# Kernel tuning notes

Hardware: AMD Instinct MI355X
Metric: run time of the kernel (lower is better)

Reference implementation:

```python
import jax, jax.numpy as jnp
import numpy as np

H = 8
D_MODEL = 1024
D_K = D_MODEL // H
NEG = -1000000000.0


def layer_norm(x, a, b, eps=1e-06):
    # torch std: unbiased (ddof=1); module divides by (std + eps)
    mean = jnp.mean(x, axis=-1, keepdims=True)
    var = jnp.sum((x - mean) ** 2, axis=-1, keepdims=True) / (x.shape[-1] - 1)
    std = jnp.sqrt(var)
    return a * (x - mean) / (std + eps) + b


def setup_inputs() -> dict:
    key = jax.random.key(0)
    ks = jax.random.split(key, 12)
    B, S, D = 8, 1024, D_MODEL
    inp = {
        "query": jax.random.normal(ks[0], (B, S, D), jnp.float32),
        "value": jax.random.normal(ks[1], (B, S, D), jnp.float32),
        "key": jax.random.normal(ks[2], (B, S, D), jnp.float32),
        "mask": jax.random.randint(ks[3], (B, S), 0, 2, jnp.int32),
        "ln_a": jnp.ones((D,), jnp.float32),
        "ln_b": jnp.zeros((D,), jnp.float32),
        "wq": jax.random.normal(ks[4], (D, D), jnp.float32) * 0.02,
        "bq": jnp.zeros((D,), jnp.float32),
        "wk": jax.random.normal(ks[5], (D, D), jnp.float32) * 0.02,
        "bk": jnp.zeros((D,), jnp.float32),
        "wv": jax.random.normal(ks[6], (D, D), jnp.float32) * 0.02,
        "bv": jnp.zeros((D,), jnp.float32),
        "w_aoa": jax.random.normal(ks[7], (2 * D, 2 * D), jnp.float32) * 0.02,  # [out, in]
        "b_aoa": jnp.zeros((2 * D,), jnp.float32),
    }
    return inp


def reference(query, value, key, mask, ln_a, ln_b, wq, bq, wk, bk, wv, bv, w_aoa, b_aoa):
    B, S, D = query.shape
    # mask [B,S] -> [B,1,1,S]
    m = mask[:, None, None, :]
    # norm_q
    q = layer_norm(query, ln_a, ln_b)
    # QKV projections, split heads -> [B,H,S,Dk]
    def split_heads(x):
        return x.reshape(B, -1, H, D_K).transpose(0, 2, 1, 3)
    q_ = split_heads(q @ wq.T + bq)
    k_ = split_heads(key @ wk.T + bk)
    v_ = split_heads(value @ wv.T + bv)
    scores = jnp.einsum("bhqd,bhkd->bhqk", q_, k_) / jnp.sqrt(jnp.float32(D_K))
    scores = jnp.where(m == 0, NEG, scores)
    p = jax.nn.softmax(scores, axis=-1)
    x = jnp.einsum("bhqk,bhkd->bhqd", p, v_)
    x = x.transpose(0, 2, 1, 3).reshape(B, S, D)
    # AoA: concat with (normed) query, linear to 2D, GLU
    z = jnp.concatenate([x, q], axis=-1) @ w_aoa.T + b_aoa
    a, g = jnp.split(z, 2, axis=-1)
    return a * jax.nn.sigmoid(g)
```

## Files before the change

kernel.cpp:

```cpp
#include <hip/hip_runtime.h>

typedef __attribute__((ext_vector_type(8))) __bf16 bf16x8;
typedef __attribute__((ext_vector_type(4))) float f32x4;

__device__ __forceinline__ ushort f2b(float f) {
    uint u = __builtin_bit_cast(uint, f);
    u += 0x7fffu + ((u >> 16) & 1u);
    return (ushort)(u >> 16);
}
__device__ __forceinline__ float b2f(ushort h) {
    uint u = ((uint)h) << 16;
    return __builtin_bit_cast(float, u);
}

__global__ __launch_bounds__(256) void cast_kernel(const float* __restrict__ src,
                                                   ushort* __restrict__ dst) {
    size_t i = ((size_t)blockIdx.x * 256 + threadIdx.x) * 4;
    float4 v = *(const float4*)(src + i);
    ushort4 o;
    o.x = f2b(v.x); o.y = f2b(v.y); o.z = f2b(v.z); o.w = f2b(v.w);
    *(ushort4*)(dst + i) = o;
}

__global__ __launch_bounds__(256) void cast_permute_aoa(const float* __restrict__ src,
                                                        ushort* __restrict__ dst) {
    int n1 = blockIdx.x >> 1;
    int c = (blockIdx.x & 1) * 1024 + threadIdx.x * 4;
    int q = ((n1 & 63) | ((n1 >> 7) << 6)) + ((n1 >> 6) & 1) * 1024;
    float4 v = *(const float4*)(src + (size_t)q * 2048 + c);
    ushort4 o;
    o.x = f2b(v.x); o.y = f2b(v.y); o.z = f2b(v.z); o.w = f2b(v.w);
    *(ushort4*)(dst + (size_t)n1 * 2048 + c) = o;
}

__global__ __launch_bounds__(256) void ln_kernel(const float* __restrict__ x,
                                                 const float* __restrict__ ga,
                                                 const float* __restrict__ be,
                                                 ushort* __restrict__ xq) {
    const int row = blockIdx.x, tid = threadIdx.x;
    __shared__ float red[4];
    float4 v = ((const float4*)(x + (size_t)row * 1024))[tid];
    float sm = v.x + v.y + v.z + v.w;
    for (int off = 32; off; off >>= 1) sm += __shfl_xor(sm, off);
    if ((tid & 63) == 0) red[tid >> 6] = sm;
    __syncthreads();
    float mean = (red[0] + red[1] + red[2] + red[3]) * (1.f / 1024.f);
    __syncthreads();
    float dx = v.x - mean, dy = v.y - mean, dz = v.z - mean, dw = v.w - mean;
    float s2 = dx * dx + dy * dy + dz * dz + dw * dw;
    for (int off = 32; off; off >>= 1) s2 += __shfl_xor(s2, off);
    if ((tid & 63) == 0) red[tid >> 6] = s2;
    __syncthreads();
    float var = (red[0] + red[1] + red[2] + red[3]) * (1.f / 1023.f);
    float inv = 1.f / (sqrtf(var) + 1e-6f);
    float4 g = ((const float4*)ga)[tid];
    float4 bb = ((const float4*)be)[tid];
    ushort4 o;
    o.x = f2b(g.x * dx * inv + bb.x);
    o.y = f2b(g.y * dy * inv + bb.y);
    o.z = f2b(g.z * dz * inv + bb.z);
    o.w = f2b(g.w * dw * inv + bb.w);
    *(ushort4*)&xq[(size_t)row * 2048 + 1024 + tid * 4] = o;
}

__global__ __launch_bounds__(256) void gemm2(const ushort* __restrict__ A, int lda,
                                             const ushort* __restrict__ B, int ldb,
                                             const float* __restrict__ bias,
                                             ushort* __restrict__ C, int ldc,
                                             int K, int NB, float scale, int mode) {
    __shared__ ushort As[2][8192];
    __shared__ ushort Bs[2][8192];
    const int tid = threadIdx.x;
    const int w = tid >> 6, l = tid & 63;
    const int wr = w >> 1, wc = w & 1;
    const int r16 = l & 15, g4 = l >> 4;

    const int bid = blockIdx.x;
    const int cpx = gridDim.x >> 3;
    const int swz = (bid & 7) * cpx + (bid >> 3);
    const int m0 = (swz / NB) * 128;
    const int n0 = (swz % NB) * 128;

    const int srow = l >> 3;
    const int scol = ((l & 7) ^ srow) * 8;
    const ushort* Asrc = A + (size_t)(m0 + w * 8 + srow) * lda + scol;
    const ushort* Bsrc = B + (size_t)(n0 + w * 8 + srow) * ldb + scol;

    f32x4 acc[4][4];
#pragma unroll
    for (int i = 0; i < 4; i++)
#pragma unroll
        for (int j = 0; j < 4; j++) acc[i][j] = (f32x4){0.f, 0.f, 0.f, 0.f};

    auto STAGE = [&](int sel, int kt) {
#pragma unroll
        for (int it = 0; it < 4; it++) {
            __builtin_amdgcn_global_load_lds(
                (const __attribute__((address_space(1))) void*)(Asrc + (size_t)(it * 32) * lda + kt * 64),
                (__attribute__((address_space(3))) void*)(&As[sel][(it * 4 + w) * 512]), 16, 0, 0);
            __builtin_amdgcn_global_load_lds(
                (const __attribute__((address_space(1))) void*)(Bsrc + (size_t)(it * 32) * ldb + kt * 64),
                (__attribute__((address_space(3))) void*)(&Bs[sel][(it * 4 + w) * 512]), 16, 0, 0);
        }
    };

    const int swzr = (g4 ^ (r16 & 7)) << 4;

    auto COMPUTE = [&](int sel, int kt, bool stage_next) {
        if (stage_next) STAGE(sel ^ 1, kt + 1);
        const char* Ab = (const char*)&As[sel][0];
        const char* Bb = (const char*)&Bs[sel][0];
        bf16x8 af[4][2], bfv[4][2];
#pragma unroll
        for (int mi = 0; mi < 4; mi++) {
            int ba = (wr * 64 + mi * 16 + r16) * 128 + swzr;
            af[mi][0] = *(const bf16x8*)(Ab + ba);
            af[mi][1] = *(const bf16x8*)(Ab + (ba ^ 64));
        }
#pragma unroll
        for (int ni = 0; ni < 4; ni++) {
            int bb = (wc * 64 + ni * 16 + r16) * 128 + swzr;
            bfv[ni][0] = *(const bf16x8*)(Bb + bb);
            bfv[ni][1] = *(const bf16x8*)(Bb + (bb ^ 64));
        }
        __builtin_amdgcn_s_setprio(1);
#pragma unroll
        for (int ks = 0; ks < 2; ks++)
#pragma unroll
            for (int mi = 0; mi < 4; mi++)
#pragma unroll
                for (int ni = 0; ni < 4; ni++)
                    acc[mi][ni] = __builtin_amdgcn_mfma_f32_16x16x32_bf16(af[mi][ks], bfv[ni][ks], acc[mi][ni], 0, 0, 0);
        __builtin_amdgcn_s_setprio(0);
        asm volatile("s_waitcnt vmcnt(0)" ::: "memory");
        __syncthreads();
    };

    STAGE(0, 0);
    asm volatile("s_waitcnt vmcnt(0)" ::: "memory");
    __syncthreads();
    const int NT = K >> 6;
    for (int kt = 0; kt < NT; kt += 2) {
        COMPUTE(0, kt, true);
        COMPUTE(1, kt + 1, kt + 2 < NT);
    }

    const int row0 = m0 + wr * 64;
    const int col0 = n0 + wc * 64;
    if (mode == 0) {
#pragma unroll
        for (int ni = 0; ni < 4; ni++) {
            int n = col0 + ni * 16 + r16;
            float bs = bias[n];
#pragma unroll
            for (int mi = 0; mi < 4; mi++) {
                int mr = row0 + mi * 16 + g4 * 4;
#pragma unroll
                for (int r = 0; r < 4; r++) {
                    C[(size_t)(mr + r) * ldc + n] = f2b((acc[mi][ni][r] + bs) * scale);
                }
            }
        }
    } else {
#pragma unroll
        for (int ni = 0; ni < 4; ni++) {
            int n = col0 + ni * 16 + r16;
            float bs = bias[n];
            int h = n >> 7, d = n & 127;
#pragma unroll
            for (int mi = 0; mi < 4; mi++) {
                int m = row0 + mi * 16 + g4 * 4;
                int b_ = m >> 10, s_ = m & 1023;
                ushort4 o;
                o.x = f2b((acc[mi][ni][0] + bs) * scale);
                o.y = f2b((acc[mi][ni][1] + bs) * scale);
                o.z = f2b((acc[mi][ni][2] + bs) * scale);
                o.w = f2b((acc[mi][ni][3] + bs) * scale);
                *(ushort4*)&C[((size_t)(b_ * 8 + h) * 128 + d) * 1024 + s_] = o;
            }
        }
    }
}

__global__ __launch_bounds__(512, 2) void gemm3(const ushort* __restrict__ A, int lda,
                                                const ushort* __restrict__ B, int ldb,
                                                const float* __restrict__ bias,
                                                float* __restrict__ out,
                                                int K, int NB) {
    __shared__ ushort lds[2][32768];

    const int tid = threadIdx.x;
    const int w = tid >> 6, l = tid & 63;
    const int wr = w >> 2, wcn = w & 3;
    const int r16 = l & 15, g4 = l >> 4;

    const int bid = blockIdx.x;
    const int cpx = gridDim.x >> 3;
    const int swz = (bid & 7) * cpx + (bid >> 3);
    const int m0 = (swz / NB) * 256;
    const int n0 = (swz % NB) * 256;

    const int srow8 = l >> 3;
    const int sxor8 = ((l & 7) ^ srow8) * 8;
    const ushort* As0 = A + (size_t)(m0 + w * 8 + srow8) * lda + sxor8;
    const ushort* Bs0 = B + (size_t)(n0 + w * 8 + srow8) * ldb + sxor8;

    f32x4 acc[8][4];
#pragma unroll
    for (int i = 0; i < 8; i++)
#pragma unroll
        for (int j = 0; j < 4; j++) acc[i][j] = (f32x4){0.f, 0.f, 0.f, 0.f};

    const int sw16 = (r16 & 7) << 4;
    char* ldsb = (char*)&lds[0][0];

#define STAGE_H(sel_, HS_, kt_)                                                            \
    do {                                                                                   \
        const int mat_ = (HS_)&1, half_ = (HS_) >> 1;                                      \
        const ushort* sb_ = mat_ ? Bs0 : As0;                                              \
        const int ld_ = mat_ ? ldb : lda;                                                  \
        _Pragma("unroll") for (int li_ = 0; li_ < 2; li_++) {                              \
            const ushort* src_ = sb_ + (size_t)(half_ * 128 + li_ * 64) * ld_ + (kt_)*64;  \
            int dst_ = (sel_)*65536 + mat_ * 32768 + half_ * 16384 + li_ * 8192 + w * 1024;\
            __builtin_amdgcn_global_load_lds(                                              \
                (const __attribute__((address_space(1))) void*)src_,                       \
                (__attribute__((address_space(3))) void*)(ldsb + dst_), 16, 0, 0);         \
        }                                                                                  \
    } while (0)

    auto LDA4 = [&](bf16x8 (&dst)[4][2], int sel, int half) {
#pragma unroll
        for (int ai = 0; ai < 4; ai++)
#pragma unroll
            for (int ks = 0; ks < 2; ks++)
                dst[ai][ks] = *(const bf16x8*)(ldsb + sel * 65536 + half * 16384 +
                                               (wr * 16 + 32 * ai + r16) * 128 +
                                               ((ks * 64 + g4 * 16) ^ sw16));
    };
    auto LDB2 = [&](bf16x8 (&dst)[2][2], int sel, int half) {
#pragma unroll
        for (int bi = 0; bi < 2; bi++)
#pragma unroll
            for (int ks = 0; ks < 2; ks++)
                dst[bi][ks] = *(const bf16x8*)(ldsb + sel * 65536 + 32768 + half * 16384 +
                                               (wcn * 16 + 64 * bi + r16) * 128 +
                                               ((ks * 64 + g4 * 16) ^ sw16));
    };
    auto MM = [&](bf16x8 (&af)[4][2], bf16x8 (&bf)[2][2], int A0, int B0) {
        __builtin_amdgcn_s_setprio(1);
#pragma unroll
        for (int ks = 0; ks < 2; ks++)
#pragma unroll
            for (int ai = 0; ai < 4; ai++)
#pragma unroll
                for (int bi = 0; bi < 2; bi++)
                    acc[A0 + ai][B0 + bi] = __builtin_amdgcn_mfma_f32_16x16x32_bf16(
                        af[ai][ks], bf[bi][ks], acc[A0 + ai][B0 + bi], 0, 0, 0);
        __builtin_amdgcn_s_setprio(0);
    };

    const int NT = K >> 6;

    STAGE_H(0, 0, 0); STAGE_H(0, 1, 0); STAGE_H(0, 2, 0); STAGE_H(0, 3, 0);
    asm volatile("s_waitcnt vmcnt(0)" ::: "memory");
    __builtin_amdgcn_s_barrier();

    bf16x8 aL[4][2], aH[4][2], bL[2][2], bH[2][2];

    for (int t = 0; t < NT; ++t) {
        const int sel = t & 1;
        const bool pf = (t + 1 < NT);
        LDA4(aL, sel, 0); LDB2(bL, sel, 0);
        if (pf) STAGE_H(sel ^ 1, 0, t + 1);
        __builtin_amdgcn_s_barrier();
        MM(aL, bL, 0, 0);
        asm volatile("s_waitcnt vmcnt(4)" ::: "memory");
        __builtin_amdgcn_s_barrier();
        LDA4(aH, sel, 1);
        if (pf) STAGE_H(sel ^ 1, 1, t + 1);
        __builtin_amdgcn_s_barrier();
        MM(aH, bL, 4, 0);
        asm volatile("s_waitcnt vmcnt(4)" ::: "memory");
        __builtin_amdgcn_s_barrier();
        LDB2(bH, sel, 1);
        if (pf) STAGE_H(sel ^ 1, 2, t + 1);
        __builtin_amdgcn_s_barrier();
        MM(aH, bH, 4, 2);
        asm volatile("s_waitcnt vmcnt(4)" ::: "memory");
        __builtin_amdgcn_s_barrier();
        if (pf) STAGE_H(sel ^ 1, 3, t + 1);
        __builtin_amdgcn_s_barrier();
        MM(aL, bH, 0, 2);
        asm volatile("s_waitcnt vmcnt(4)" ::: "memory");
        __builtin_amdgcn_s_barrier();
    }
#undef STAGE_H

#pragma unroll
    for (int bp = 0; bp < 2; bp++) {
        int j = (n0 >> 1) + wcn * 16 + 64 * bp + r16;
        float bsa = bias[j];
        float bsg = bias[j + 1024];
#pragma unroll
        for (int a_ = 0; a_ < 8; a_++) {
            int mr = m0 + wr * 16 + 32 * a_ + g4 * 4;
#pragma unroll
            for (int r = 0; r < 4; r++) {
                float av = acc[a_][2 * bp][r] + bsa;
                float gv = acc[a_][2 * bp + 1][r] + bsg;
                out[(size_t)(mr + r) * 1024 + j] = av * (1.f / (1.f + __expf(-gv)));
            }
        }
    }
}

__global__ __launch_bounds__(512, 4) void attn_kernel(const ushort* __restrict__ Q,
                                                      const ushort* __restrict__ Kt,
                                                      const ushort* __restrict__ Vt,
                                                      const int* __restrict__ mask,
                                                      ushort* __restrict__ xq) {
    __shared__ ushort Ks[2][8192];
    __shared__ ushort Vs[2][8192];
    __shared__ ushort Pl[8][1024];

    const int tid = threadIdx.x;
    const int l = tid & 63, wid = tid >> 6;
    const int r16 = l & 15, g4 = l >> 4;
    const int id = blockIdx.x;
    const int bh = ((id >> 6) << 3) | (id & 7);
    const int qb = (id >> 3) & 7;
    const int b = bh >> 3, h = bh & 7;
    const int q0 = qb * 128 + wid * 16;

    bf16x8 qf[4];
    const ushort* Qrow = Q + (size_t)(b * 1024 + q0 + r16) * 1024 + h * 128 + g4 * 8;
#pragma unroll
    for (int kf = 0; kf < 4; kf++) qf[kf] = *(const bf16x8*)(Qrow + kf * 32);

    const ushort* Kg = Kt + ((size_t)b * 1024) * 1024 + h * 128;
    const ushort* Vg = Vt + (size_t)(b * 8 + h) * 128 * 1024;
    const int* mptr = mask + b * 1024;

    f32x4 xacc[8];
#pragma unroll
    for (int i = 0; i < 8; i++) xacc[i] = (f32x4){0.f, 0.f, 0.f, 0.f};
    float mrow = -INFINITY, lrow = 0.f, sclp = 0.f;

    char* Pme = (char*)&Pl[wid][0];
    const int pswz = (r16 & 7) << 4;

    auto STAGE_K = [&](int sel, int t) {
        const int kv0 = t * 64;
#pragma unroll
        for (int it = 0; it < 2; ++it) {
            int ob = it * 8192 + wid * 1024;
            int o = ob + l * 16;
            int row = o >> 8;
            int sc = (o & 255) ^ ((row & 7) << 4);
            const ushort* src = Kg + (size_t)(kv0 + row) * 1024 + (sc >> 1);
            __builtin_amdgcn_global_load_lds((const __attribute__((address_space(1))) void*)src,
                (__attribute__((address_space(3))) void*)((char*)&Ks[sel][0] + ob), 16, 0, 0);
        }
    };
    auto STAGE_V = [&](int sel, int t) {
        const int kv0 = t * 64;
#pragma unroll
        for (int it = 0; it < 2; ++it) {
            int ob = it * 8192 + wid * 1024;
            int o = ob + l * 16;
            int d = o >> 7;
            int sc = (o & 127) ^ ((d & 7) << 4);
            const ushort* src = Vg + (size_t)d * 1024 + kv0 + (sc >> 1);
            __builtin_amdgcn_global_load_lds((const __attribute__((address_space(1))) void*)src,
                (__attribute__((address_space(3))) void*)((char*)&Vs[sel][0] + ob), 16, 0, 0);
        }
    };

    auto QK = [&](f32x4 (&s)[4], int sel, unsigned long long wt) {
        const char* Kb_ = (const char*)&Ks[sel][0];
#pragma unroll
        for (int cg = 0; cg < 4; cg++) {
            s[cg] = (f32x4){0.f, 0.f, 0.f, 0.f};
            const int rowk = cg * 16 + r16;
            const char* kr = Kb_ + rowk * 256;
            const int sw = (rowk & 7) << 4;
            __builtin_amdgcn_s_setprio(1);
#pragma unroll
            for (int kf = 0; kf < 4; kf++) {
                bf16x8 kfr = *(const bf16x8*)(kr + ((kf * 64 + g4 * 16) ^ sw));
                s[cg] = __builtin_amdgcn_mfma_f32_16x16x32_bf16(kfr, qf[kf], s[cg], 0, 0, 0);
            }
            __builtin_amdgcn_s_setprio(0);
            uint nib = (uint)(wt >> (cg * 16 + g4 * 4)) & 15u;
#pragma unroll
            for (int r = 0; r < 4; r++)
                if (!((nib >> r) & 1u)) s[cg][r] = -1e9f;
        }
    };
    auto PV = [&](int sel) {
        const char* Vb_ = (const char*)&Vs[sel][0];
        bf16x8 pfr[2];
#pragma unroll
        for (int ks = 0; ks < 2; ks++)
            pfr[ks] = *(const bf16x8*)(Pme + r16 * 128 + ((g4 * 16 + ks * 64) ^ pswz));
#pragma unroll
        for (int cg2 = 0; cg2 < 8; cg2++)
#pragma unroll
            for (int r = 0; r < 4; r++) xacc[cg2][r] *= sclp;
        __builtin_amdgcn_s_setprio(1);
#pragma unroll
        for (int ks = 0; ks < 2; ks++) {
#pragma unroll
            for (int cg2 = 0; cg2 < 8; cg2++) {
                const int d = cg2 * 16 + r16;
                bf16x8 vfr = *(const bf16x8*)(Vb_ + d * 128 + ((ks * 64 + g4 * 16) ^ ((d & 7) << 4)));
                xacc[cg2] = __builtin_amdgcn_mfma_f32_16x16x32_bf16(vfr, pfr[ks], xacc[cg2], 0, 0, 0);
            }
        }
        __builtin_amdgcn_s_setprio(0);
    };
    auto SOFTMAX = [&](f32x4 (&s)[4]) {
        float pmax = -INFINITY;
#pragma unroll
        for (int cg = 0; cg < 4; cg++)
#pragma unroll
            for (int r = 0; r < 4; r++) pmax = fmaxf(pmax, s[cg][r]);
        pmax = fmaxf(pmax, __shfl_xor(pmax, 16));
        pmax = fmaxf(pmax, __shfl_xor(pmax, 32));
        float mn = fmaxf(mrow, pmax);
        sclp = __expf(mrow - mn);
        mrow = mn;
        float rsum = 0.f;
#pragma unroll
        for (int cg = 0; cg < 4; cg++)
#pragma unroll
            for (int r = 0; r < 4; r++) {
                float p = __expf(s[cg][r] - mn);
                s[cg][r] = p;
                rsum += p;
            }
        rsum += __shfl_xor(rsum, 16);
        rsum += __shfl_xor(rsum, 32);
        lrow = lrow * sclp + rsum;
#pragma unroll
        for (int cg = 0; cg < 4; cg++) {
            uint lo = ((uint)f2b(s[cg][1]) << 16) | f2b(s[cg][0]);
            uint hi = ((uint)f2b(s[cg][3]) << 16) | f2b(s[cg][2]);
            uint2 pk; pk.x = lo; pk.y = hi;
            *(uint2*)(Pme + r16 * 128 + ((cg * 32 + g4 * 8) ^ pswz)) = pk;
        }
    };

    STAGE_K(0, 0);
    int mv = mptr[l];
    asm volatile("s_waitcnt vmcnt(0)" ::: "memory");
    __syncthreads();
    STAGE_K(1, 1);
    STAGE_V(0, 0);
    unsigned long long wt = __ballot(mv != 0);
    mv = mptr[64 + l];
    {
        f32x4 s0[4];
        QK(s0, 0, wt);
        SOFTMAX(s0);
    }
    int kc = 1, vc = 0;

    for (int u = 1; u < 16; ++u) {
        wt = __ballot(mv != 0);
        asm volatile("s_waitcnt vmcnt(0)" ::: "memory");
        __syncthreads();
        if (u < 15) STAGE_K(kc ^ 1, u + 1);
        STAGE_V(vc ^ 1, u);
        if (u < 15) mv = mptr[(u + 1) * 64 + l];

        f32x4 sn[4];
        QK(sn, kc, wt);
        PV(vc);
        SOFTMAX(sn);

        kc ^= 1; vc ^= 1;
    }

    asm volatile("s_waitcnt vmcnt(0)" ::: "memory");
    __syncthreads();
    PV(vc);

    const float inv = 1.f / lrow;
    const size_t orow = (size_t)(b * 1024 + q0 + r16) * 2048 + h * 128;
#pragma unroll
    for (int cg2 = 0; cg2 < 8; cg2++) {
#pragma unroll
        for (int r = 0; r < 4; r++) {
            xq[orow + cg2 * 16 + g4 * 4 + r] = f2b(xacc[cg2][r] * inv);
        }
    }
}

extern "C" void kernel_launch(void* const* d_in, const int* in_sizes, int n_in,
                              void* d_out, int out_size, void* d_ws, size_t ws_size,
                              hipStream_t stream) {
    const float* query = (const float*)d_in[0];
    const float* value = (const float*)d_in[1];
    const float* key   = (const float*)d_in[2];
    const int*   mask  = (const int*)d_in[3];
    const float* ln_a  = (const float*)d_in[4];
    const float* ln_b  = (const float*)d_in[5];
    const float* wq    = (const float*)d_in[6];
    const float* bq    = (const float*)d_in[7];
    const float* wk    = (const float*)d_in[8];
    const float* bk    = (const float*)d_in[9];
    const float* wv    = (const float*)d_in[10];
    const float* bv    = (const float*)d_in[11];
    const float* waoa  = (const float*)d_in[12];
    const float* baoa  = (const float*)d_in[13];
    float* out = (float*)d_out;

    char* w8 = (char*)d_ws;
    ushort* xq   = (ushort*)(w8);
    ushort* Qb   = (ushort*)(w8 + 33554432);
    ushort* Kb   = (ushort*)(w8 + 50331648);
    ushort* Vt   = (ushort*)(w8 + 67108864);
    ushort* keyb = (ushort*)(w8 + 83886080);
    ushort* valb = (ushort*)(w8 + 100663296);
    ushort* wqb  = (ushort*)(w8 + 117440512);
    ushort* wkb  = (ushort*)(w8 + 119537664);
    ushort* wvb  = (ushort*)(w8 + 121634816);
    ushort* wab  = (ushort*)(w8 + 123731968);

    cast_kernel<<<8192, 256, 0, stream>>>(key, keyb);
    cast_kernel<<<8192, 256, 0, stream>>>(value, valb);
    cast_kernel<<<1024, 256, 0, stream>>>(wq, wqb);
    cast_kernel<<<1024, 256, 0, stream>>>(wk, wkb);
    cast_kernel<<<1024, 256, 0, stream>>>(wv, wvb);
    cast_permute_aoa<<<4096, 256, 0, stream>>>(waoa, wab);
    ln_kernel<<<8192, 256, 0, stream>>>(query, ln_a, ln_b, xq);

    const float qscale = 0.08838834764831845f;
    gemm2<<<512, 256, 0, stream>>>(xq + 1024, 2048, wqb, 1024, bq, Qb, 1024, 1024, 8, qscale, 0);
    gemm2<<<512, 256, 0, stream>>>(keyb, 1024, wkb, 1024, bk, Kb, 1024, 1024, 8, 1.f, 0);
    gemm2<<<512, 256, 0, stream>>>(valb, 1024, wvb, 1024, bv, Vt, 0, 1024, 8, 1.f, 1);

    attn_kernel<<<512, 512, 0, stream>>>(Qb, Kb, Vt, mask, xq);

    gemm3<<<256, 512, 0, stream>>>(xq, 2048, wab, 2048, baoa, out, 2048, 8);
}
```

Measured before the change: 242.6 us.

## Fuse QKV projections into one 256x256-tile GEMM and restage prefetch pipeline

Replaces the three separate 128x128-tile QKV GEMM launches with one templated 256x256-tile kernel. The kernel picks the A operand, bias, scale and output layout per column region of the contiguous Wq|Wk|Wv weight block. The shared GEMM main loop now issues the whole next k-tile prefetch at once, with fewer waits and barriers, and peels the last iteration so it needs no prefetch check. The aim is to cut launch count, raise operand reuse and shorten pipeline stalls. The cost is a 384-block grid that may fill the CUs unevenly, and the new loop ordering also affects the final AoA GEMM.

```diff
diff --git a/kernel.cpp b/kernel.cpp
--- a/kernel.cpp
+++ b/kernel.cpp
@@ -63,130 +63,18 @@
     *(ushort4*)&xq[(size_t)row * 2048 + 1024 + tid * 4] = o;
 }
 
-__global__ __launch_bounds__(256) void gemm2(const ushort* __restrict__ A, int lda,
-                                             const ushort* __restrict__ B, int ldb,
-                                             const float* __restrict__ bias,
-                                             ushort* __restrict__ C, int ldc,
-                                             int K, int NB, float scale, int mode) {
-    __shared__ ushort As[2][8192];
-    __shared__ ushort Bs[2][8192];
-    const int tid = threadIdx.x;
-    const int w = tid >> 6, l = tid & 63;
-    const int wr = w >> 1, wc = w & 1;
-    const int r16 = l & 15, g4 = l >> 4;
-
-    const int bid = blockIdx.x;
-    const int cpx = gridDim.x >> 3;
-    const int swz = (bid & 7) * cpx + (bid >> 3);
-    const int m0 = (swz / NB) * 128;
-    const int n0 = (swz % NB) * 128;
-
-    const int srow = l >> 3;
-    const int scol = ((l & 7) ^ srow) * 8;
-    const ushort* Asrc = A + (size_t)(m0 + w * 8 + srow) * lda + scol;
-    const ushort* Bsrc = B + (size_t)(n0 + w * 8 + srow) * ldb + scol;
-
-    f32x4 acc[4][4];
-#pragma unroll
-    for (int i = 0; i < 4; i++)
-#pragma unroll
-        for (int j = 0; j < 4; j++) acc[i][j] = (f32x4){0.f, 0.f, 0.f, 0.f};
-
-    auto STAGE = [&](int sel, int kt) {
-#pragma unroll
-        for (int it = 0; it < 4; it++) {
-            __builtin_amdgcn_global_load_lds(
-                (const __attribute__((address_space(1))) void*)(Asrc + (size_t)(it * 32) * lda + kt * 64),
-                (__attribute__((address_space(3))) void*)(&As[sel][(it * 4 + w) * 512]), 16, 0, 0);
-            __builtin_amdgcn_global_load_lds(
-                (const __attribute__((address_space(1))) void*)(Bsrc + (size_t)(it * 32) * ldb + kt * 64),
-                (__attribute__((address_space(3))) void*)(&Bs[sel][(it * 4 + w) * 512]), 16, 0, 0);
-        }
-    };
-
-    const int swzr = (g4 ^ (r16 & 7)) << 4;
-
-    auto COMPUTE = [&](int sel, int kt, bool stage_next) {
-        if (stage_next) STAGE(sel ^ 1, kt + 1);
-        const char* Ab = (const char*)&As[sel][0];
-        const char* Bb = (const char*)&Bs[sel][0];
-        bf16x8 af[4][2], bfv[4][2];
-#pragma unroll
-        for (int mi = 0; mi < 4; mi++) {
-            int ba = (wr * 64 + mi * 16 + r16) * 128 + swzr;
-            af[mi][0] = *(const bf16x8*)(Ab + ba);
-            af[mi][1] = *(const bf16x8*)(Ab + (ba ^ 64));
-        }
-#pragma unroll
-        for (int ni = 0; ni < 4; ni++) {
-            int bb = (wc * 64 + ni * 16 + r16) * 128 + swzr;
-            bfv[ni][0] = *(const bf16x8*)(Bb + bb);
-            bfv[ni][1] = *(const bf16x8*)(Bb + (bb ^ 64));
-        }
-        __builtin_amdgcn_s_setprio(1);
-#pragma unroll
-        for (int ks = 0; ks < 2; ks++)
-#pragma unroll
-            for (int mi = 0; mi < 4; mi++)
-#pragma unroll
-                for (int ni = 0; ni < 4; ni++)
-                    acc[mi][ni] = __builtin_amdgcn_mfma_f32_16x16x32_bf16(af[mi][ks], bfv[ni][ks], acc[mi][ni], 0, 0, 0);
-        __builtin_amdgcn_s_setprio(0);
-        asm volatile("s_waitcnt vmcnt(0)" ::: "memory");
-        __syncthreads();
-    };
-
-    STAGE(0, 0);
-    asm volatile("s_waitcnt vmcnt(0)" ::: "memory");
-    __syncthreads();
-    const int NT = K >> 6;
-    for (int kt = 0; kt < NT; kt += 2) {
-        COMPUTE(0, kt, true);
-        COMPUTE(1, kt + 1, kt + 2 < NT);
-    }
-
-    const int row0 = m0 + wr * 64;
-    const int col0 = n0 + wc * 64;
-    if (mode == 0) {
-#pragma unroll
-        for (int ni = 0; ni < 4; ni++) {
-            int n = col0 + ni * 16 + r16;
-            float bs = bias[n];
-#pragma unroll
-            for (int mi = 0; mi < 4; mi++) {
-                int mr = row0 + mi * 16 + g4 * 4;
-#pragma unroll
-                for (int r = 0; r < 4; r++) {
-                    C[(size_t)(mr + r) * ldc + n] = f2b((acc[mi][ni][r] + bs) * scale);
-                }
-            }
-        }
-    } else {
-#pragma unroll
-        for (int ni = 0; ni < 4; ni++) {
-            int n = col0 + ni * 16 + r16;
-            float bs = bias[n];
-            int h = n >> 7, d = n & 127;
-#pragma unroll
-            for (int mi = 0; mi < 4; mi++) {
-                int m = row0 + mi * 16 + g4 * 4;
-                int b_ = m >> 10, s_ = m & 1023;
-                ushort4 o;
-                o.x = f2b((acc[mi][ni][0] + bs) * scale);
-                o.y = f2b((acc[mi][ni][1] + bs) * scale);
-                o.z = f2b((acc[mi][ni][2] + bs) * scale);
-                o.w = f2b((acc[mi][ni][3] + bs) * scale);
-                *(ushort4*)&C[((size_t)(b_ * 8 + h) * 128 + d) * 1024 + s_] = o;
-            }
-        }
-    }
-}
-
-__global__ __launch_bounds__(512, 2) void gemm3(const ushort* __restrict__ A, int lda,
+template <int MODE>
+__global__ __launch_bounds__(512, 2) void gemm4(const ushort* __restrict__ Aq, int ldaq,
+                                                const ushort* __restrict__ Ak,
+                                                const ushort* __restrict__ Av,
                                                 const ushort* __restrict__ B, int ldb,
-                                                const float* __restrict__ bias,
-                                                float* __restrict__ out,
-                                                int K, int NB) {
+                                                const float* __restrict__ bias0,
+                                                const float* __restrict__ bias1,
+                                                const float* __restrict__ bias2,
+                                                void* __restrict__ out0,
+                                                void* __restrict__ out1,
+                                                void* __restrict__ out2,
+                                                int K, int NB, float qscale) {
     __shared__ ushort lds[2][32768];
 
     const int tid = threadIdx.x;
@@ -200,6 +88,10 @@
     const int m0 = (swz / NB) * 256;
     const int n0 = (swz % NB) * 256;
 
+    const int region = (MODE == 0) ? (n0 >> 10) : 0;
+    const ushort* A = (MODE == 0) ? (region == 0 ? Aq : (region == 1 ? Ak : Av)) : Aq;
+    const int lda = (MODE == 0) ? (region == 0 ? ldaq : 1024) : ldaq;
+
     const int srow8 = l >> 3;
     const int sxor8 = ((l & 7) ^ srow8) * 8;
     const ushort* As0 = A + (size_t)(m0 + w * 8 + srow8) * lda + sxor8;
@@ -214,19 +106,30 @@
     const int sw16 = (r16 & 7) << 4;
     char* ldsb = (char*)&lds[0][0];
 
-#define STAGE_H(sel_, HS_, kt_)                                                            \
-    do {                                                                                   \
-        const int mat_ = (HS_)&1, half_ = (HS_) >> 1;                                      \
-        const ushort* sb_ = mat_ ? Bs0 : As0;                                              \
-        const int ld_ = mat_ ? ldb : lda;                                                  \
-        _Pragma("unroll") for (int li_ = 0; li_ < 2; li_++) {                              \
-            const ushort* src_ = sb_ + (size_t)(half_ * 128 + li_ * 64) * ld_ + (kt_)*64;  \
-            int dst_ = (sel_)*65536 + mat_ * 32768 + half_ * 16384 + li_ * 8192 + w * 1024;\
-            __builtin_amdgcn_global_load_lds(                                              \
-                (const __attribute__((address_space(1))) void*)src_,                       \
-                (__attribute__((address_space(3))) void*)(ldsb + dst_), 16, 0, 0);         \
-        }                                                                                  \
-    } while (0)
+#define GL16(src_, dst_)                                                        \
+    __builtin_amdgcn_global_load_lds(                                           \
+        (const __attribute__((address_space(1))) void*)(src_),                  \
+        (__attribute__((address_space(3))) void*)(dst_), 16, 0, 0)
+
+    auto STAGE8 = [&](int sel, int kt) {
+        const size_t ko = (size_t)kt * 64;
+#pragma unroll
+        for (int li = 0; li < 2; li++)
+            GL16(As0 + (size_t)(li * 64) * lda + ko,
+                 ldsb + sel * 65536 + li * 8192 + w * 1024);
+#pragma unroll
+        for (int li = 0; li < 2; li++)
+            GL16(Bs0 + (size_t)(li * 64) * ldb + ko,
+                 ldsb + sel * 65536 + 32768 + li * 8192 + w * 1024);
+#pragma unroll
+        for (int li = 0; li < 2; li++)
+            GL16(As0 + (size_t)(128 + li * 64) * lda + ko,
+                 ldsb + sel * 65536 + 16384 + li * 8192 + w * 1024);
+#pragma unroll
+        for (int li = 0; li < 2; li++)
+            GL16(Bs0 + (size_t)(128 + li * 64) * ldb + ko,
+                 ldsb + sel * 65536 + 32768 + 16384 + li * 8192 + w * 1024);
+    };
 
     auto LDA4 = [&](bf16x8 (&dst)[4][2], int sel, int half) {
 #pragma unroll
@@ -261,54 +164,101 @@
 
     const int NT = K >> 6;
 
-    STAGE_H(0, 0, 0); STAGE_H(0, 1, 0); STAGE_H(0, 2, 0); STAGE_H(0, 3, 0);
+    STAGE8(0, 0);
     asm volatile("s_waitcnt vmcnt(0)" ::: "memory");
     __builtin_amdgcn_s_barrier();
 
     bf16x8 aL[4][2], aH[4][2], bL[2][2], bH[2][2];
 
-    for (int t = 0; t < NT; ++t) {
+    for (int t = 0; t < NT - 1; ++t) {
         const int sel = t & 1;
-        const bool pf = (t + 1 < NT);
         LDA4(aL, sel, 0); LDB2(bL, sel, 0);
-        if (pf) STAGE_H(sel ^ 1, 0, t + 1);
+        STAGE8(sel ^ 1, t + 1);
         __builtin_amdgcn_s_barrier();
         MM(aL, bL, 0, 0);
-        asm volatile("s_waitcnt vmcnt(4)" ::: "memory");
+        asm volatile("s_waitcnt vmcnt(8)" ::: "memory");
         __builtin_amdgcn_s_barrier();
         LDA4(aH, sel, 1);
-        if (pf) STAGE_H(sel ^ 1, 1, t + 1);
         __builtin_amdgcn_s_barrier();
         MM(aH, bL, 4, 0);
-        asm volatile("s_waitcnt vmcnt(4)" ::: "memory");
         __builtin_amdgcn_s_barrier();
         LDB2(bH, sel, 1);
-        if (pf) STAGE_H(sel ^ 1, 2, t + 1);
         __builtin_amdgcn_s_barrier();
         MM(aH, bH, 4, 2);
-        asm volatile("s_waitcnt vmcnt(4)" ::: "memory");
-        __builtin_amdgcn_s_barrier();
-        if (pf) STAGE_H(sel ^ 1, 3, t + 1);
         __builtin_amdgcn_s_barrier();
         MM(aL, bH, 0, 2);
         asm volatile("s_waitcnt vmcnt(4)" ::: "memory");
         __builtin_amdgcn_s_barrier();
     }
-#undef STAGE_H
-
-#pragma unroll
-    for (int bp = 0; bp < 2; bp++) {
-        int j = (n0 >> 1) + wcn * 16 + 64 * bp + r16;
-        float bsa = bias[j];
-        float bsg = bias[j + 1024];
-#pragma unroll
-        for (int a_ = 0; a_ < 8; a_++) {
-            int mr = m0 + wr * 16 + 32 * a_ + g4 * 4;
-#pragma unroll
-            for (int r = 0; r < 4; r++) {
-                float av = acc[a_][2 * bp][r] + bsa;
-                float gv = acc[a_][2 * bp + 1][r] + bsg;
-                out[(size_t)(mr + r) * 1024 + j] = av * (1.f / (1.f + __expf(-gv)));
+    {
+        const int sel = (NT - 1) & 1;
+        LDA4(aL, sel, 0); LDB2(bL, sel, 0);
+        __builtin_amdgcn_s_barrier();
+        MM(aL, bL, 0, 0);
+        asm volatile("s_waitcnt vmcnt(0)" ::: "memory");
+        __builtin_amdgcn_s_barrier();
+        LDA4(aH, sel, 1);
+        LDB2(bH, sel, 1);
+        MM(aH, bL, 4, 0);
+        MM(aH, bH, 4, 2);
+        MM(aL, bH, 0, 2);
+    }
+#undef GL16
+
+    if (MODE == 1) {
+        float* out = (float*)out0;
+#pragma unroll
+        for (int bp = 0; bp < 2; bp++) {
+            int j = (n0 >> 1) + wcn * 16 + 64 * bp + r16;
+            float bsa = bias0[j];
+            float bsg = bias0[j + 1024];
+#pragma unroll
+            for (int a_ = 0; a_ < 8; a_++) {
+                int mr = m0 + wr * 16 + 32 * a_ + g4 * 4;
+#pragma unroll
+                for (int r = 0; r < 4; r++) {
+                    float av = acc[a_][2 * bp][r] + bsa;
+                    float gv = acc[a_][2 * bp + 1][r] + bsg;
+                    out[(size_t)(mr + r) * 1024 + j] = av * (1.f / (1.f + __expf(-gv)));
+                }
+            }
+        }
+    } else {
+        const int nr0 = n0 & 1023;
+        const float* bias = region == 0 ? bias0 : (region == 1 ? bias1 : bias2);
+        const float scale = region == 0 ? qscale : 1.f;
+        if (region < 2) {
+            ushort* C = (ushort*)(region == 0 ? out0 : out1);
+#pragma unroll
+            for (int b_ = 0; b_ < 4; b_++) {
+                int n = nr0 + wcn * 16 + 64 * b_ + r16;
+                float bs = bias[n];
+#pragma unroll
+                for (int a_ = 0; a_ < 8; a_++) {
+                    int mr = m0 + wr * 16 + 32 * a_ + g4 * 4;
+#pragma unroll
+                    for (int r = 0; r < 4; r++)
+                        C[(size_t)(mr + r) * 1024 + n] = f2b((acc[a_][b_][r] + bs) * scale);
+                }
+            }
+        } else {
+            ushort* Vt = (ushort*)out2;
+#pragma unroll
+            for (int b_ = 0; b_ < 4; b_++) {
+                int n = nr0 + wcn * 16 + 64 * b_ + r16;
+                float bs = bias[n];
+                int h = n >> 7, d = n & 127;
+#pragma unroll
+                for (int a_ = 0; a_ < 8; a_++) {
+                    int mr = m0 + wr * 16 + 32 * a_ + g4 * 4;
+                    int bb = mr >> 10, s_ = mr & 1023;
+                    ushort4 o;
+                    o.x = f2b(acc[a_][b_][0] + bs);
+                    o.y = f2b(acc[a_][b_][1] + bs);
+                    o.z = f2b(acc[a_][b_][2] + bs);
+                    o.w = f2b(acc[a_][b_][3] + bs);
+                    *(ushort4*)&Vt[((size_t)(bb * 8 + h) * 128 + d) * 1024 + s_] = o;
+                }
             }
         }
     }
@@ -537,11 +487,14 @@
     ln_kernel<<<8192, 256, 0, stream>>>(query, ln_a, ln_b, xq);
 
     const float qscale = 0.08838834764831845f;
-    gemm2<<<512, 256, 0, stream>>>(xq + 1024, 2048, wqb, 1024, bq, Qb, 1024, 1024, 8, qscale, 0);
-    gemm2<<<512, 256, 0, stream>>>(keyb, 1024, wkb, 1024, bk, Kb, 1024, 1024, 8, 1.f, 0);
-    gemm2<<<512, 256, 0, stream>>>(valb, 1024, wvb, 1024, bv, Vt, 0, 1024, 8, 1.f, 1);
+
+    gemm4<0><<<384, 512, 0, stream>>>(xq + 1024, 2048, keyb, valb,
+                                      wqb, 1024, bq, bk, bv,
+                                      Qb, Kb, Vt, 1024, 12, qscale);
 
     attn_kernel<<<512, 512, 0, stream>>>(Qb, Kb, Vt, mask, xq);
 
-    gemm3<<<256, 512, 0, stream>>>(xq, 2048, wab, 2048, baoa, out, 2048, 8);
-}
+    gemm4<1><<<256, 512, 0, stream>>>(xq, 2048, nullptr, nullptr,
+                                      wab, 2048, baoa, nullptr, nullptr,
+                                      out, nullptr, nullptr, 2048, 8, 1.f);
+}
```

After: 241.4 us. About the same (-0.5%).
